# Kernel tuning notes

Measured on AMD Instinct MI355X. Metric: run time of the kernel, lower is better.

The kernel has to match this reference:

```python
import jax, jax.numpy as jnp
import numpy as np

B, T, C = 8, 2048, 1024
H, D = 16, 64
DLOW = 64  # D_DECAY = D_AAA = D_MV = D_GATE = 64
EPS_LN = 1e-5


def setup_inputs() -> dict:
    key = jax.random.key(0)
    ks = jax.random.split(key, 26)
    p = lambda k, shape, s=0.02: (jax.random.normal(k, shape, jnp.float32) * s)
    u = lambda k, shape: jax.random.uniform(k, shape, jnp.float32)
    return {
        "x":   jax.random.normal(ks[0], (B, T, C), jnp.float32),
        # token-shift mix coefficients (1,1,C)
        "x_r": u(ks[1], (1, 1, C)), "x_w": u(ks[2], (1, 1, C)),
        "x_k": u(ks[3], (1, 1, C)), "x_v": u(ks[4], (1, 1, C)),
        "x_a": u(ks[5], (1, 1, C)), "x_g": u(ks[6], (1, 1, C)),
        # decay lora: w1 [C,DLOW], w2 [DLOW,H], w0 [1,1,H,1]
        "w0": p(ks[7], (1, 1, H, 1)), "w1": p(ks[8], (C, DLOW)), "w2": p(ks[9], (DLOW, H)),
        # in-context lr lora
        "a0": p(ks[10], (1, 1, H, 1)), "a1": p(ks[11], (C, DLOW)), "a2": p(ks[12], (DLOW, H)),
        # value residual lora
        "v0": p(ks[13], (1, 1, C)), "v1": p(ks[14], (C, DLOW)), "v2": p(ks[15], (DLOW, C)),
        # gate lora
        "g1": p(ks[16], (C, DLOW)), "g2": p(ks[17], (DLOW, C)),
        "k_k": 0.85 + p(ks[18], (1, 1, C)),
        "r_k": p(ks[19], (H, D)),
        # main projections, stored [in, out] so x @ W matches nn.Linear
        "Wr": p(ks[20], (C, C)), "Wk": p(ks[21], (C, C)),
        "Wv": p(ks[22], (C, C)), "Wo": p(ks[23], (C, C)),
        # GroupNorm(n_head, n_embd) affine params
        "ln_w": jnp.ones((C,), jnp.float32) + p(ks[24], (C,)),
        "ln_b": p(ks[25], (C,)),
    }


def reference(x, x_r, x_w, x_k, x_v, x_a, x_g,
              w0, w1, w2, a0, a1, a2, v0, v1, v2, g1, g2,
              k_k, r_k, Wr, Wk, Wv, Wo, ln_w, ln_b):
    Bb, Tt, Cc = x.shape
    Hh, Dd = r_k.shape
    # token shift: sx = x_t - x_{t-1} (zero-padded)
    xx = jnp.concatenate([jnp.zeros((Bb, 1, Cc), x.dtype), x[:, :-1]], axis=1)
    sx = x - xx
    xr = x + sx * x_r
    xw = x + sx * x_w
    xk = x + sx * x_k
    xv = x + sx * x_v
    xa = x + sx * x_a
    xg = x + sx * x_g

    r = (xr @ Wr).reshape(Bb, Tt, Hh, Dd)
    # decay in (0, exp(-0.5)): exp(-softplus(-(w0 + lora)) - 0.5)
    w = jnp.exp(-jax.nn.softplus(-(w0 + (jnp.tanh(xw @ w1) @ w2).reshape(Bb, Tt, Hh, 1))) - 0.5)
    k = xk @ Wk
    v = xv @ Wv
    v_res_gate = jax.nn.sigmoid(v0 + jnp.tanh(xv @ v1) @ v2)
    v = v + (v - v) * v_res_gate  # no-op, kept for faithfulness
    a = jax.nn.sigmoid(a0 + (jnp.tanh(xa @ a1) @ a2).reshape(Bb, Tt, Hh, 1))
    g = jax.nn.sigmoid(jnp.tanh(xg @ g1) @ g2)

    kk = (k * k_k).reshape(Bb, Tt, Hh, Dd)
    kk = kk / jnp.maximum(jnp.linalg.norm(kk, axis=-1, keepdims=True), 1e-12)
    vh = v.reshape(Bb, Tt, Hh, Dd)

    # WKV linear recurrence: state = state * w_t + kk_t * v_t * a_t
    kv = (kk * vh * a).astype(jnp.float32)            # [B,T,H,D]
    w_t = jnp.moveaxis(w.astype(jnp.float32), 1, 0)   # [T,B,H,1]
    kv_t = jnp.moveaxis(kv, 1, 0)                     # [T,B,H,D]

    def step(state, inputs):
        wt, kvt = inputs
        state = state * wt + kvt
        return state, state

    init = jnp.zeros((Bb, Hh, Dd), jnp.float32)
    _, states = jax.lax.scan(step, init, (w_t, kv_t))  # [T,B,H,D]
    x_wkv = jnp.moveaxis(states, 0, 1).astype(x.dtype)  # [B,T,H,D]

    x_wkv = x_wkv * r
    bonus = jnp.sum(r * kk * r_k, axis=-1, keepdims=True) * vh
    x_wkv = x_wkv + bonus  # [B,T,H,D]

    # GroupNorm(H groups over C channels), per (B*T) sample
    mean = x_wkv.mean(axis=-1, keepdims=True)
    var = x_wkv.var(axis=-1, keepdims=True)
    xn = (x_wkv - mean) * jax.lax.rsqrt(var + EPS_LN)
    xn = xn.reshape(Bb, Tt, Cc) * ln_w + ln_b

    return (xn * g) @ Wo
```

## Files before the change

kernel.cpp:

```cpp
#include <hip/hip_runtime.h>


typedef __bf16 bf16;
typedef __attribute__((ext_vector_type(8))) __bf16 bf16x8;
typedef __attribute__((ext_vector_type(4))) float f32x4;

#define TBTOK 16384
#define TSEQ  2048
#define CDIM  1024
#define HN    16
#define CHUNK 32
#define NCH   64

__device__ __forceinline__ float wredsum(float v) {
#pragma unroll
  for (int o = 32; o > 0; o >>= 1) v += __shfl_xor(v, o, 64);
  return v;
}
__device__ __forceinline__ float redsum8(float v) {
#pragma unroll
  for (int o = 4; o > 0; o >>= 1) v += __shfl_xor(v, o, 64);
  return v;
}
__device__ __forceinline__ float sigmf(float x) { return 1.f / (1.f + expf(-x)); }

__device__ __forceinline__ void gl_lds16(const bf16* g, bf16* l) {
  __builtin_amdgcn_global_load_lds(
      (const __attribute__((address_space(1))) unsigned int*)g,
      (__attribute__((address_space(3))) unsigned int*)l, 16, 0, 0);
}

__global__ __launch_bounds__(256) void prep_kern(
    const float* __restrict__ x, const float* __restrict__ mr,
    const float* __restrict__ mk, const float* __restrict__ mv,
    bf16* __restrict__ xr, bf16* __restrict__ xk, bf16* __restrict__ xv,
    bf16* __restrict__ xbf,
    const float* __restrict__ Wr, const float* __restrict__ Wk,
    const float* __restrict__ Wv, const float* __restrict__ Wo,
    const float* __restrict__ w1, const float* __restrict__ a1, const float* __restrict__ g1,
    const float* __restrict__ mw, const float* __restrict__ ma, const float* __restrict__ mg,
    const float* __restrict__ g2, const float* __restrict__ w2, const float* __restrict__ a2,
    bf16* __restrict__ WrT, bf16* __restrict__ WkT, bf16* __restrict__ WvT, bf16* __restrict__ WoT,
    bf16* __restrict__ Bcat, bf16* __restrict__ g2T,
    bf16* __restrict__ w2T, bf16* __restrict__ a2T, float* __restrict__ zpad) {
  int bid0 = blockIdx.x;
  int tid = threadIdx.x;
  if (bid0 < 8192) {
    long i8 = ((long)bid0 * 256 + tid) * 8;
    int m = (int)(i8 >> 10);
    int c = (int)(i8 & 1023);
    f32x4 x0 = *(const f32x4*)(x + i8);
    f32x4 x1 = *(const f32x4*)(x + i8 + 4);
    f32x4 p0 = {0.f, 0.f, 0.f, 0.f}, p1 = {0.f, 0.f, 0.f, 0.f};
    if ((m & (TSEQ - 1)) != 0) {
      p0 = *(const f32x4*)(x + i8 - CDIM);
      p1 = *(const f32x4*)(x + i8 - CDIM + 4);
    }
    f32x4 r0 = *(const f32x4*)(mr + c), r1 = *(const f32x4*)(mr + c + 4);
    f32x4 k0 = *(const f32x4*)(mk + c), k1 = *(const f32x4*)(mk + c + 4);
    f32x4 v0 = *(const f32x4*)(mv + c), v1 = *(const f32x4*)(mv + c + 4);
    bf16x8 or_, ok_, ov_, ox_;
#pragma unroll
    for (int j = 0; j < 4; j++) {
      float s0 = x0[j] - p0[j], s1 = x1[j] - p1[j];
      or_[j] = (bf16)(x0[j] + s0 * r0[j]); or_[4 + j] = (bf16)(x1[j] + s1 * r1[j]);
      ok_[j] = (bf16)(x0[j] + s0 * k0[j]); ok_[4 + j] = (bf16)(x1[j] + s1 * k1[j]);
      ov_[j] = (bf16)(x0[j] + s0 * v0[j]); ov_[4 + j] = (bf16)(x1[j] + s1 * v1[j]);
      ox_[j] = (bf16)x0[j];                ox_[4 + j] = (bf16)x1[j];
    }
    *(bf16x8*)(xr + i8) = or_;
    *(bf16x8*)(xk + i8) = ok_;
    *(bf16x8*)(xv + i8) = ov_;
    *(bf16x8*)(xbf + i8) = ox_;
    return;
  }
  int bid = bid0 - 8192;
  int tx = tid & 31, ty = tid >> 5;
  __shared__ bf16 tile[32][33];
  if (bid < 4096) {
    int sel = bid >> 10, t = bid & 1023;
    int k0 = (t >> 5) * 32, n0 = (t & 31) * 32;
    const float* src = sel == 0 ? Wr : (sel == 1 ? Wk : (sel == 2 ? Wv : Wo));
    bf16* dst = sel == 0 ? WrT : (sel == 1 ? WkT : (sel == 2 ? WvT : WoT));
#pragma unroll
    for (int i = 0; i < 4; i++)
      tile[ty + i * 8][tx] = (bf16)src[(long)(k0 + ty + i * 8) * 1024 + n0 + tx];
    __syncthreads();
#pragma unroll
    for (int i = 0; i < 4; i++)
      dst[(long)(n0 + ty + i * 8) * 1024 + k0 + tx] = tile[tx][ty + i * 8];
  } else if (bid < 4480) {
    int idx = bid - 4096;
    int mat = idx >> 7, rem = idx & 127;
    int half = rem >> 6, t = rem & 63;
    int k0 = (t >> 1) * 32, n0 = (t & 1) * 32;
    const float* W = mat == 0 ? w1 : (mat == 1 ? a1 : g1);
    const float* mx = mat == 0 ? mw : (mat == 1 ? ma : mg);
#pragma unroll
    for (int i = 0; i < 4; i++) {
      int k = k0 + ty + i * 8;
      float s = half == 0 ? (1.f + mx[k]) : (-mx[k]);
      tile[ty + i * 8][tx] = (bf16)(s * W[(long)k * 64 + n0 + tx]);
    }
    __syncthreads();
#pragma unroll
    for (int i = 0; i < 4; i++)
      Bcat[(long)(mat * 64 + n0 + ty + i * 8) * 2048 + half * 1024 + k0 + tx] =
          tile[tx][ty + i * 8];
  } else if (bid < 4544) {
    int t = bid - 4480;
    int k0 = (t >> 5) * 32, n0 = (t & 31) * 32;
#pragma unroll
    for (int i = 0; i < 4; i++)
      tile[ty + i * 8][tx] = (bf16)g2[(long)(k0 + ty + i * 8) * 1024 + n0 + tx];
    __syncthreads();
#pragma unroll
    for (int i = 0; i < 4; i++)
      g2T[(long)(n0 + ty + i * 8) * 64 + k0 + tx] = tile[tx][ty + i * 8];
  } else {
#pragma unroll
    for (int rep = 0; rep < 4; rep++) {
      int idx = rep * 256 + tid;
      int k = idx >> 4, h = idx & 15;
      w2T[h * 64 + k] = (bf16)w2[idx];
      a2T[h * 64 + k] = (bf16)a2[idx];
    }
    if (tid < 64) zpad[tid] = 0.f;
  }
}

template <int ACT, typename OT>
__global__ __launch_bounds__(256) void gemm128_kern(
    const bf16* __restrict__ A0, const bf16* __restrict__ A1, const bf16* __restrict__ A2,
    int apitch,
    const bf16* __restrict__ BT0, const bf16* __restrict__ BT1, const bf16* __restrict__ BT2,
    OT* __restrict__ out0, OT* __restrict__ out1, OT* __restrict__ out2,
    int opitch, int K, int nbpm) {
  int bx = blockIdx.x;
  int mat = bx / nbpm;
  int ncol0 = (bx % nbpm) * 128;
  const bf16* Am = mat == 0 ? A0 : (mat == 1 ? A1 : A2);
  const bf16* BTm = mat == 0 ? BT0 : (mat == 1 ? BT1 : BT2);
  OT* out = mat == 0 ? out0 : (mat == 1 ? out1 : out2);
  int m0 = blockIdx.y * 128;

  __shared__ bf16 Al[128 * 64];
  __shared__ bf16 Bl[128 * 64];

  int tid = threadIdx.x;
  int w = tid >> 6, lane = tid & 63, quad = lane >> 4, lr = lane & 15;
  int wm = (w & 1) * 64, wn = (w >> 1) * 64;

  f32x4 acc[4][4] = {};

  int r0 = tid >> 3;
  int slot = tid & 7;
  int kg = (slot ^ (r0 & 7)) * 8;
  const bf16* ag = Am + (long)(m0 + r0) * apitch + kg;
  const bf16* bg = BTm + (long)(ncol0 + r0) * K + kg;
  long astep = (long)32 * apitch;
  long bstep = (long)32 * K;
  bf16* la = Al + w * 512;
  bf16* lb = Bl + w * 512;

  for (int k0 = 0; k0 < K; k0 += 64) {
#pragma unroll
    for (int s = 0; s < 4; s++) gl_lds16(ag + s * astep, la + s * 2048);
#pragma unroll
    for (int s = 0; s < 4; s++) gl_lds16(bg + s * bstep, lb + s * 2048);
    ag += 64; bg += 64;
    __syncthreads();
#pragma unroll
    for (int ko = 0; ko < 2; ko++) {
      bf16x8 af[4], bff[4];
#pragma unroll
      for (int i = 0; i < 4; i++) {
        int ra = wm + i * 16 + lr;
        af[i] = *(const bf16x8*)&Al[ra * 64 + (((ko * 4 + quad) ^ (ra & 7)) * 8)];
      }
#pragma unroll
      for (int j = 0; j < 4; j++) {
        int rb = wn + j * 16 + lr;
        bff[j] = *(const bf16x8*)&Bl[rb * 64 + (((ko * 4 + quad) ^ (rb & 7)) * 8)];
      }
#pragma unroll
      for (int i = 0; i < 4; i++)
#pragma unroll
        for (int j = 0; j < 4; j++)
          acc[i][j] = __builtin_amdgcn_mfma_f32_16x16x32_bf16(af[i], bff[j], acc[i][j], 0, 0, 0);
    }
    __syncthreads();
  }
#pragma unroll
  for (int i = 0; i < 4; i++)
#pragma unroll
    for (int j = 0; j < 4; j++)
#pragma unroll
      for (int rg = 0; rg < 4; rg++) {
        int row = m0 + wm + i * 16 + quad * 4 + rg;
        int col = ncol0 + wn + j * 16 + lr;
        float v = acc[i][j][rg];
        if (ACT == 1) v = sigmf(v);
        out[(long)row * opitch + col] = (OT)v;
      }
}

__global__ __launch_bounds__(256) void stage1_kern(
    const bf16* __restrict__ xbf, const bf16* __restrict__ Bcat,
    const float* __restrict__ zpad, const bf16* __restrict__ w2T, const bf16* __restrict__ a2T,
    const float* __restrict__ w0, const float* __restrict__ a0,
    bf16* __restrict__ t1g, float* __restrict__ w_arr, float* __restrict__ a_arr) {
  int m0 = blockIdx.x * 64;
  int part = blockIdx.y;
  __shared__ bf16 Al[64 * 32];
  __shared__ bf16 Bl[128 * 32];
  __shared__ bf16 Lt1[64 * 136];

  int tid = threadIdx.x;
  int w = tid >> 6, lane = tid & 63, quad = lane >> 4, lr = lane & 15;
  int wm = w * 16;

  int r0 = tid >> 2, kc0 = (tid & 3) * 8;
  int m = m0 + r0;
  const bf16* asrc = xbf + (long)m * CDIM + kc0;
  bool firstrow = (m & (TSEQ - 1)) == 0;
  const bf16* psrc = firstrow ? (const bf16*)zpad : xbf + (long)(m - 1) * CDIM + kc0;
  int pstep = firstrow ? 0 : 32;
  int brow0 = part ? 128 : 0;
  const bf16* bs0 = Bcat + (long)(brow0 + r0) * 2048 + kc0;
  const bf16* bs1 = bs0 + (long)64 * 2048;
  bf16* la = Al + w * 512;
  bf16* lb0 = Bl + w * 512;
  bf16* lb1 = Bl + 2048 + w * 512;

  if (part == 0) {
    f32x4 acc[8] = {};
#pragma unroll 1
    for (int kk = 0; kk < 64; kk++) {
      if (kk < 32) { gl_lds16(asrc, la); asrc += 32; }
      else         { gl_lds16(psrc, la); psrc += pstep; }
      gl_lds16(bs0, lb0);
      gl_lds16(bs1, lb1);
      bs0 += 32; bs1 += 32;
      __syncthreads();
      bf16x8 af = *(const bf16x8*)&Al[(wm + lr) * 32 + quad * 8];
#pragma unroll
      for (int nf = 0; nf < 8; nf++) {
        bf16x8 bff = *(const bf16x8*)&Bl[(nf * 16 + lr) * 32 + quad * 8];
        acc[nf] = __builtin_amdgcn_mfma_f32_16x16x32_bf16(af, bff, acc[nf], 0, 0, 0);
      }
      __syncthreads();
    }
#pragma unroll
    for (int nf = 0; nf < 8; nf++)
#pragma unroll
      for (int rg = 0; rg < 4; rg++) {
        int row = wm + quad * 4 + rg;
        Lt1[row * 136 + nf * 16 + lr] = (bf16)tanhf(acc[nf][rg]);
      }
    __syncthreads();
#pragma unroll
    for (int rep = 0; rep < 4; rep++) {
      int idx = rep * 256 + tid;
      int row = idx >> 4, h = idx & 15;
      const bf16* rw = &Lt1[row * 136];
      const bf16* ra = rw + 64;
      const bf16* ww = w2T + h * 64;
      const bf16* aw = a2T + h * 64;
      float dw = 0.f, da = 0.f;
#pragma unroll
      for (int k = 0; k < 64; k++) {
        dw += (float)rw[k] * (float)ww[k];
        da += (float)ra[k] * (float)aw[k];
      }
      w_arr[h * TBTOK + m0 + row] = 0.60653066f * sigmf(w0[h] + dw);
      a_arr[h * TBTOK + m0 + row] = sigmf(a0[h] + da);
    }
  } else {
    f32x4 acc[4] = {};
#pragma unroll 1
    for (int kk = 0; kk < 64; kk++) {
      if (kk < 32) { gl_lds16(asrc, la); asrc += 32; }
      else         { gl_lds16(psrc, la); psrc += pstep; }
      gl_lds16(bs0, lb0);
      bs0 += 32;
      __syncthreads();
      bf16x8 af = *(const bf16x8*)&Al[(wm + lr) * 32 + quad * 8];
#pragma unroll
      for (int nf = 0; nf < 4; nf++) {
        bf16x8 bff = *(const bf16x8*)&Bl[(nf * 16 + lr) * 32 + quad * 8];
        acc[nf] = __builtin_amdgcn_mfma_f32_16x16x32_bf16(af, bff, acc[nf], 0, 0, 0);
      }
      __syncthreads();
    }
#pragma unroll
    for (int nf = 0; nf < 4; nf++)
#pragma unroll
      for (int rg = 0; rg < 4; rg++) {
        int row = wm + quad * 4 + rg;
        t1g[(long)(m0 + row) * 64 + nf * 16 + lr] = (bf16)tanhf(acc[nf][rg]);
      }
  }
}

__global__ __launch_bounds__(256) void scan1_kern(
    const bf16* __restrict__ k_buf, const bf16* __restrict__ v_buf, const bf16* __restrict__ r_buf,
    const float* __restrict__ k_k, const float* __restrict__ r_k,
    const float* __restrict__ a_arr, const float* __restrict__ w_arr,
    float* __restrict__ kv2, float* __restrict__ Parr, float* __restrict__ bonus,
    float* __restrict__ Lend) {
  int wid = blockIdx.x * 4 + (threadIdx.x >> 6);
  int lane = threadIdx.x & 63;
  int bh = wid >> 6, c = wid & 63;
  int b = bh >> 4, h = bh & 15;
  int mstart = b * TSEQ + c * CHUNK;
  int kc = h * 64 + lane;
  float kkc = k_k[kc], rkc = r_k[kc];
  float st = 0.f, cw = 1.f;
  long mbase = (long)mstart * CDIM + kc;
  int hm = h * TBTOK + mstart;
  long sbase = ((long)hm) * 64 + lane;
  float kf = (float)k_buf[mbase] * kkc;
  float vf = (float)v_buf[mbase];
  float rf = (float)r_buf[mbase];
  float af = a_arr[hm];
  float wt = w_arr[hm];
  for (int t = 0; t < CHUNK; t++) {
    float kf_n = 0.f, vf_n = 0.f, rf_n = 0.f, af_n = 0.f, wt_n = 0.f;
    if (t < CHUNK - 1) {
      kf_n = (float)k_buf[mbase + CDIM] * kkc;
      vf_n = (float)v_buf[mbase + CDIM];
      rf_n = (float)r_buf[mbase + CDIM];
      af_n = a_arr[hm + 1];
      wt_n = w_arr[hm + 1];
    }
    float ss = wredsum(kf * kf);
    float kkn = kf / fmaxf(sqrtf(ss), 1e-12f);
    st = st * wt + kkn * vf * af;
    kv2[sbase] = st;
    cw *= wt;
    float bs = wredsum(rf * kkn * rkc);
    if (lane == 0) {
      Parr[hm] = cw;
      bonus[(mstart + t) * HN + h] = bs;
    }
    kf = kf_n; vf = vf_n; rf = rf_n; af = af_n; wt = wt_n;
    mbase += CDIM; hm += 1; sbase += 64;
  }
  Lend[(long)wid * 64 + lane] = st;
}

__global__ __launch_bounds__(256) void gate_post_kern(
    const bf16* __restrict__ t1g, const bf16* __restrict__ g2T,
    const float* __restrict__ kv2, const float* __restrict__ Parr,
    const float* __restrict__ Lend, const float* __restrict__ bonus,
    bf16* __restrict__ r_buf, const bf16* __restrict__ v_buf,
    const float* __restrict__ ln_w, const float* __restrict__ ln_b) {
  int ncol0 = blockIdx.x * 128;
  int m0 = blockIdx.y * 128;

  __shared__ bf16 Al[128 * 32];
  __shared__ bf16 Bl[128 * 32];
  __shared__ bf16 gtile[128 * 136];

  int tid = threadIdx.x;
  int w = tid >> 6, lane = tid & 63, quad = lane >> 4, lr = lane & 15;
  int wm = (w & 1) * 64, wn = (w >> 1) * 64;

  f32x4 acc[4][4] = {};

  int r0 = tid >> 2, kc0 = (tid & 3) * 8;
  const bf16* ag0 = t1g + (long)(m0 + r0) * 64 + kc0;
  const bf16* ag1 = ag0 + (long)64 * 64;
  const bf16* bg0 = g2T + (long)(ncol0 + r0) * 64 + kc0;
  const bf16* bg1 = bg0 + (long)64 * 64;
  bf16* la0 = Al + w * 512;
  bf16* la1 = Al + 2048 + w * 512;
  bf16* lb0 = Bl + w * 512;
  bf16* lb1 = Bl + 2048 + w * 512;

  for (int k0 = 0; k0 < 64; k0 += 32) {
    gl_lds16(ag0, la0);
    gl_lds16(ag1, la1);
    gl_lds16(bg0, lb0);
    gl_lds16(bg1, lb1);
    ag0 += 32; ag1 += 32; bg0 += 32; bg1 += 32;
    __syncthreads();
    bf16x8 af[4], bff[4];
#pragma unroll
    for (int i = 0; i < 4; i++) af[i] = *(const bf16x8*)&Al[(wm + i * 16 + lr) * 32 + quad * 8];
#pragma unroll
    for (int j = 0; j < 4; j++) bff[j] = *(const bf16x8*)&Bl[(wn + j * 16 + lr) * 32 + quad * 8];
#pragma unroll
    for (int i = 0; i < 4; i++)
#pragma unroll
      for (int j = 0; j < 4; j++)
        acc[i][j] = __builtin_amdgcn_mfma_f32_16x16x32_bf16(af[i], bff[j], acc[i][j], 0, 0, 0);
    __syncthreads();
  }
#pragma unroll
  for (int i = 0; i < 4; i++)
#pragma unroll
    for (int j = 0; j < 4; j++)
#pragma unroll
      for (int rg = 0; rg < 4; rg++) {
        int row = wm + i * 16 + quad * 4 + rg;
        int col = wn + j * 16 + lr;
        gtile[row * 136 + col] = (bf16)sigmf(acc[i][j][rg]);
      }
  __syncthreads();

  int c_loc = (tid & 15) * 8;
  int col_g = ncol0 + c_loc;
  int h = col_g >> 6;
  int d0 = col_g & 63;
  f32x4 lnw0 = *(const f32x4*)(ln_w + col_g);
  f32x4 lnw1 = *(const f32x4*)(ln_w + col_g + 4);
  f32x4 lnb0 = *(const f32x4*)(ln_b + col_g);
  f32x4 lnb1 = *(const f32x4*)(ln_b + col_g + 4);
#pragma unroll
  for (int jj = 0; jj < 8; jj++) {
    int row = jj * 16 + (tid >> 4);
    int row_g = m0 + row;
    int b = row_g >> 11;
    int ch = (row_g & (TSEQ - 1)) >> 5;
    long kvb = ((long)h * TBTOK + row_g) * 64 + d0;
    f32x4 st0 = *(const f32x4*)(kv2 + kvb);
    f32x4 st1 = *(const f32x4*)(kv2 + kvb + 4);
    f32x4 cy0 = {0.f, 0.f, 0.f, 0.f}, cy1 = {0.f, 0.f, 0.f, 0.f};
    if (ch != 0) {
      long lb = ((long)((b * 16 + h) * NCH + ch - 1)) * 64 + d0;
      cy0 = *(const f32x4*)(Lend + lb);
      cy1 = *(const f32x4*)(Lend + lb + 4);
    }
    float pw = Parr[h * TBTOK + row_g];
    float bs = bonus[row_g * HN + h];
    long rb = (long)row_g * CDIM + col_g;
    bf16x8 rf8 = *(const bf16x8*)(r_buf + rb);
    bf16x8 vf8 = *(const bf16x8*)(v_buf + rb);
    bf16x8 g8 = *(const bf16x8*)&gtile[row * 136 + c_loc];
    float xw[8];
#pragma unroll
    for (int q = 0; q < 4; q++) {
      xw[q]     = (st0[q] + pw * cy0[q]) * (float)rf8[q]     + bs * (float)vf8[q];
      xw[4 + q] = (st1[q] + pw * cy1[q]) * (float)rf8[4 + q] + bs * (float)vf8[4 + q];
    }
    float sum = 0.f;
#pragma unroll
    for (int q = 0; q < 8; q++) sum += xw[q];
    float mn = redsum8(sum) * (1.f / 64.f);
    float vs = 0.f;
#pragma unroll
    for (int q = 0; q < 8; q++) {
      xw[q] -= mn;
      vs += xw[q] * xw[q];
    }
    float var = redsum8(vs) * (1.f / 64.f);
    float rq = rsqrtf(var + 1e-5f);
    bf16x8 o8;
#pragma unroll
    for (int q = 0; q < 4; q++) {
      o8[q]     = (bf16)((xw[q] * rq * lnw0[q] + lnb0[q]) * (float)g8[q]);
      o8[4 + q] = (bf16)((xw[4 + q] * rq * lnw1[q] + lnb1[q]) * (float)g8[4 + q]);
    }
    *(bf16x8*)(r_buf + rb) = o8;
  }
}

extern "C" void kernel_launch(void* const* d_in, const int* in_sizes, int n_in,
                              void* d_out, int out_size, void* d_ws, size_t ws_size,
                              hipStream_t stream) {
  const float* x    = (const float*)d_in[0];
  const float* x_r  = (const float*)d_in[1];
  const float* x_w  = (const float*)d_in[2];
  const float* x_k  = (const float*)d_in[3];
  const float* x_v  = (const float*)d_in[4];
  const float* x_a  = (const float*)d_in[5];
  const float* x_g  = (const float*)d_in[6];
  const float* w0   = (const float*)d_in[7];
  const float* w1   = (const float*)d_in[8];
  const float* w2   = (const float*)d_in[9];
  const float* a0   = (const float*)d_in[10];
  const float* a1   = (const float*)d_in[11];
  const float* a2   = (const float*)d_in[12];
  const float* g1   = (const float*)d_in[16];
  const float* g2   = (const float*)d_in[17];
  const float* k_k  = (const float*)d_in[18];
  const float* r_k  = (const float*)d_in[19];
  const float* Wr   = (const float*)d_in[20];
  const float* Wk   = (const float*)d_in[21];
  const float* Wv   = (const float*)d_in[22];
  const float* Wo   = (const float*)d_in[23];
  const float* ln_w = (const float*)d_in[24];
  const float* ln_b = (const float*)d_in[25];
  float* out = (float*)d_out;

  char* p = (char*)d_ws;
  auto carve = [&](size_t bytes) {
    void* r = (void*)p;
    p += (bytes + 255) & ~(size_t)255;
    return r;
  };
  bf16* WrT = (bf16*)carve(1024 * 1024 * 2);
  bf16* WkT = (bf16*)carve(1024 * 1024 * 2);
  bf16* WvT = (bf16*)carve(1024 * 1024 * 2);
  bf16* WoT = (bf16*)carve(1024 * 1024 * 2);
  bf16* Bcat = (bf16*)carve(192 * 2048 * 2);
  bf16* g2T  = (bf16*)carve(1024 * 64 * 2);
  bf16* w2T  = (bf16*)carve(16 * 64 * 2);
  bf16* a2T  = (bf16*)carve(16 * 64 * 2);
  float* zpad = (float*)carve(64 * 4);
  bf16* t1g   = (bf16*)carve((size_t)TBTOK * 64 * 2);
  bf16* r_buf = (bf16*)carve((size_t)TBTOK * CDIM * 2);
  bf16* k_buf = (bf16*)carve((size_t)TBTOK * CDIM * 2);
  bf16* v_buf = (bf16*)carve((size_t)TBTOK * CDIM * 2);
  float* w_arr = (float*)carve((size_t)TBTOK * HN * 4);
  float* a_arr = (float*)carve((size_t)TBTOK * HN * 4);
  float* bonus = (float*)carve((size_t)TBTOK * HN * 4);
  float* Parr  = (float*)carve((size_t)TBTOK * HN * 4);
  float* Lend  = (float*)carve((size_t)128 * NCH * 64 * 4);
  bf16* xr  = (bf16*)carve((size_t)TBTOK * CDIM * 2);
  bf16* xk  = (bf16*)carve((size_t)TBTOK * CDIM * 2);
  bf16* xv  = (bf16*)carve((size_t)TBTOK * CDIM * 2);
  bf16* xbf = (bf16*)carve((size_t)TBTOK * CDIM * 2);
  float* kv2 = (float*)xv;

  prep_kern<<<dim3(8192 + 4545), 256, 0, stream>>>(
      x, x_r, x_k, x_v, xr, xk, xv, xbf,
      Wr, Wk, Wv, Wo, w1, a1, g1, x_w, x_a, x_g, g2, w2, a2,
      WrT, WkT, WvT, WoT, Bcat, g2T, w2T, a2T, zpad);
  stage1_kern<<<dim3(TBTOK / 64, 2), 256, 0, stream>>>(
      xbf, Bcat, zpad, w2T, a2T, w0, a0, t1g, w_arr, a_arr);
  gemm128_kern<0, bf16><<<dim3(24, TBTOK / 128), 256, 0, stream>>>(
      xr, xk, xv, CDIM, WrT, WkT, WvT,
      r_buf, k_buf, v_buf, CDIM, 1024, 8);
  scan1_kern<<<dim3(128 * NCH / 4), 256, 0, stream>>>(
      k_buf, v_buf, r_buf, k_k, r_k, a_arr, w_arr, kv2, Parr, bonus, Lend);
  gate_post_kern<<<dim3(8, TBTOK / 128), 256, 0, stream>>>(
      t1g, g2T, kv2, Parr, Lend, bonus, r_buf, v_buf, ln_w, ln_b);
  gemm128_kern<0, float><<<dim3(8, TBTOK / 128), 256, 0, stream>>>(
      r_buf, r_buf, r_buf, CDIM, WoT, WoT, WoT,
      out, out, out, CDIM, 1024, 8);
}
```

Before: 569.1 us.

## Merge stage1 with RKV GEMM launch, store scan states in bf16, fuse reductions

Folds the stage1 LoRA kernel and the R/K/V projection GEMM into one launch: grid rows 0-3 do stage1 work and the rest do GEMM tiles, so the two independent kernels can overlap. The scan kernel now writes per-step states as bf16 instead of fp32, halving that intermediate's write and read traffic at some precision cost. It also combines the two wave reductions (key norm and bonus) into one shuffle loop. The Wo GEMM gets a dedicated kernel with the grid swapped so blocks sharing a row tile run close together.

```diff
diff --git a/kernel.cpp b/kernel.cpp
--- a/kernel.cpp
+++ b/kernel.cpp
@@ -12,11 +12,6 @@
 #define CHUNK 32
 #define NCH   64
 
-__device__ __forceinline__ float wredsum(float v) {
-#pragma unroll
-  for (int o = 32; o > 0; o >>= 1) v += __shfl_xor(v, o, 64);
-  return v;
-}
 __device__ __forceinline__ float redsum8(float v) {
 #pragma unroll
   for (int o = 4; o > 0; o >>= 1) v += __shfl_xor(v, o, 64);
@@ -129,97 +124,87 @@
   }
 }
 
-template <int ACT, typename OT>
-__global__ __launch_bounds__(256) void gemm128_kern(
-    const bf16* __restrict__ A0, const bf16* __restrict__ A1, const bf16* __restrict__ A2,
-    int apitch,
-    const bf16* __restrict__ BT0, const bf16* __restrict__ BT1, const bf16* __restrict__ BT2,
-    OT* __restrict__ out0, OT* __restrict__ out1, OT* __restrict__ out2,
-    int opitch, int K, int nbpm) {
-  int bx = blockIdx.x;
-  int mat = bx / nbpm;
-  int ncol0 = (bx % nbpm) * 128;
-  const bf16* Am = mat == 0 ? A0 : (mat == 1 ? A1 : A2);
-  const bf16* BTm = mat == 0 ? BT0 : (mat == 1 ? BT1 : BT2);
-  OT* out = mat == 0 ? out0 : (mat == 1 ? out1 : out2);
-  int m0 = blockIdx.y * 128;
-
-  __shared__ bf16 Al[128 * 64];
-  __shared__ bf16 Bl[128 * 64];
-
-  int tid = threadIdx.x;
-  int w = tid >> 6, lane = tid & 63, quad = lane >> 4, lr = lane & 15;
-  int wm = (w & 1) * 64, wn = (w >> 1) * 64;
-
-  f32x4 acc[4][4] = {};
-
-  int r0 = tid >> 3;
-  int slot = tid & 7;
-  int kg = (slot ^ (r0 & 7)) * 8;
-  const bf16* ag = Am + (long)(m0 + r0) * apitch + kg;
-  const bf16* bg = BTm + (long)(ncol0 + r0) * K + kg;
-  long astep = (long)32 * apitch;
-  long bstep = (long)32 * K;
-  bf16* la = Al + w * 512;
-  bf16* lb = Bl + w * 512;
-
-  for (int k0 = 0; k0 < K; k0 += 64) {
-#pragma unroll
-    for (int s = 0; s < 4; s++) gl_lds16(ag + s * astep, la + s * 2048);
-#pragma unroll
-    for (int s = 0; s < 4; s++) gl_lds16(bg + s * bstep, lb + s * 2048);
-    ag += 64; bg += 64;
-    __syncthreads();
-#pragma unroll
-    for (int ko = 0; ko < 2; ko++) {
-      bf16x8 af[4], bff[4];
-#pragma unroll
-      for (int i = 0; i < 4; i++) {
-        int ra = wm + i * 16 + lr;
-        af[i] = *(const bf16x8*)&Al[ra * 64 + (((ko * 4 + quad) ^ (ra & 7)) * 8)];
-      }
-#pragma unroll
-      for (int j = 0; j < 4; j++) {
-        int rb = wn + j * 16 + lr;
-        bff[j] = *(const bf16x8*)&Bl[rb * 64 + (((ko * 4 + quad) ^ (rb & 7)) * 8)];
-      }
-#pragma unroll
-      for (int i = 0; i < 4; i++)
-#pragma unroll
-        for (int j = 0; j < 4; j++)
-          acc[i][j] = __builtin_amdgcn_mfma_f32_16x16x32_bf16(af[i], bff[j], acc[i][j], 0, 0, 0);
-    }
-    __syncthreads();
-  }
-#pragma unroll
-  for (int i = 0; i < 4; i++)
-#pragma unroll
-    for (int j = 0; j < 4; j++)
-#pragma unroll
-      for (int rg = 0; rg < 4; rg++) {
-        int row = m0 + wm + i * 16 + quad * 4 + rg;
-        int col = ncol0 + wn + j * 16 + lr;
-        float v = acc[i][j][rg];
-        if (ACT == 1) v = sigmf(v);
-        out[(long)row * opitch + col] = (OT)v;
-      }
-}
-
-__global__ __launch_bounds__(256) void stage1_kern(
+__global__ __launch_bounds__(256) void rkv_stage1_kern(
+    const bf16* __restrict__ xr, const bf16* __restrict__ xk, const bf16* __restrict__ xv,
+    const bf16* __restrict__ WrT, const bf16* __restrict__ WkT, const bf16* __restrict__ WvT,
+    bf16* __restrict__ r_buf, bf16* __restrict__ k_buf, bf16* __restrict__ v_buf,
     const bf16* __restrict__ xbf, const bf16* __restrict__ Bcat,
     const float* __restrict__ zpad, const bf16* __restrict__ w2T, const bf16* __restrict__ a2T,
     const float* __restrict__ w0, const float* __restrict__ a0,
     bf16* __restrict__ t1g, float* __restrict__ w_arr, float* __restrict__ a_arr) {
-  int m0 = blockIdx.x * 64;
-  int part = blockIdx.y;
-  __shared__ bf16 Al[64 * 32];
-  __shared__ bf16 Bl[128 * 32];
-  __shared__ bf16 Lt1[64 * 136];
-
+  __shared__ __align__(16) char smem[32768];
   int tid = threadIdx.x;
   int w = tid >> 6, lane = tid & 63, quad = lane >> 4, lr = lane & 15;
+  int y = blockIdx.y;
+
+  if (y >= 4) {
+    int yy = y - 4;
+    int mat = yy >> 3;
+    int ncol0 = (yy & 7) * 128;
+    const bf16* Am = mat == 0 ? xr : (mat == 1 ? xk : xv);
+    const bf16* BTm = mat == 0 ? WrT : (mat == 1 ? WkT : WvT);
+    bf16* out = mat == 0 ? r_buf : (mat == 1 ? k_buf : v_buf);
+    int m0 = blockIdx.x * 128;
+    bf16* Al = (bf16*)smem;
+    bf16* Bl = (bf16*)(smem + 16384);
+    int wm = (w & 1) * 64, wn = (w >> 1) * 64;
+    f32x4 acc[4][4] = {};
+    int r0 = tid >> 3;
+    int slot = tid & 7;
+    int kg = (slot ^ (r0 & 7)) * 8;
+    const bf16* ag = Am + (long)(m0 + r0) * CDIM + kg;
+    const bf16* bg = BTm + (long)(ncol0 + r0) * 1024 + kg;
+    long astep = (long)32 * CDIM;
+    long bstep = (long)32 * 1024;
+    bf16* la = Al + w * 512;
+    bf16* lb = Bl + w * 512;
+    for (int k0 = 0; k0 < 1024; k0 += 64) {
+#pragma unroll
+      for (int s = 0; s < 4; s++) gl_lds16(ag + s * astep, la + s * 2048);
+#pragma unroll
+      for (int s = 0; s < 4; s++) gl_lds16(bg + s * bstep, lb + s * 2048);
+      ag += 64; bg += 64;
+      __syncthreads();
+#pragma unroll
+      for (int ko = 0; ko < 2; ko++) {
+        bf16x8 af[4], bff[4];
+#pragma unroll
+        for (int i = 0; i < 4; i++) {
+          int ra = wm + i * 16 + lr;
+          af[i] = *(const bf16x8*)&Al[ra * 64 + (((ko * 4 + quad) ^ (ra & 7)) * 8)];
+        }
+#pragma unroll
+        for (int j = 0; j < 4; j++) {
+          int rb = wn + j * 16 + lr;
+          bff[j] = *(const bf16x8*)&Bl[rb * 64 + (((ko * 4 + quad) ^ (rb & 7)) * 8)];
+        }
+#pragma unroll
+        for (int i = 0; i < 4; i++)
+#pragma unroll
+          for (int j = 0; j < 4; j++)
+            acc[i][j] = __builtin_amdgcn_mfma_f32_16x16x32_bf16(af[i], bff[j], acc[i][j], 0, 0, 0);
+      }
+      __syncthreads();
+    }
+#pragma unroll
+    for (int i = 0; i < 4; i++)
+#pragma unroll
+      for (int j = 0; j < 4; j++)
+#pragma unroll
+        for (int rg = 0; rg < 4; rg++) {
+          int row = m0 + wm + i * 16 + quad * 4 + rg;
+          int col = ncol0 + wn + j * 16 + lr;
+          out[(long)row * CDIM + col] = (bf16)acc[i][j][rg];
+        }
+    return;
+  }
+
+  int part = y >> 1;
+  int m0 = blockIdx.x * 128 + (y & 1) * 64;
+  bf16* Al = (bf16*)smem;
+  bf16* Bl = (bf16*)(smem + 4096);
+  bf16* Lt1 = (bf16*)(smem + 12288);
   int wm = w * 16;
-
   int r0 = tid >> 2, kc0 = (tid & 3) * 8;
   int m = m0 + r0;
   const bf16* asrc = xbf + (long)m * CDIM + kc0;
@@ -303,11 +288,70 @@
   }
 }
 
+__global__ __launch_bounds__(256) void gemm_wo_kern(
+    const bf16* __restrict__ A, const bf16* __restrict__ BT, float* __restrict__ out) {
+  int ncol0 = blockIdx.y * 128;
+  int m0 = blockIdx.x * 128;
+  __shared__ bf16 Al[128 * 64];
+  __shared__ bf16 Bl[128 * 64];
+  int tid = threadIdx.x;
+  int w = tid >> 6, lane = tid & 63, quad = lane >> 4, lr = lane & 15;
+  int wm = (w & 1) * 64, wn = (w >> 1) * 64;
+  f32x4 acc[4][4] = {};
+  int r0 = tid >> 3;
+  int slot = tid & 7;
+  int kg = (slot ^ (r0 & 7)) * 8;
+  const bf16* ag = A + (long)(m0 + r0) * CDIM + kg;
+  const bf16* bg = BT + (long)(ncol0 + r0) * 1024 + kg;
+  long astep = (long)32 * CDIM;
+  long bstep = (long)32 * 1024;
+  bf16* la = Al + w * 512;
+  bf16* lb = Bl + w * 512;
+  for (int k0 = 0; k0 < 1024; k0 += 64) {
+#pragma unroll
+    for (int s = 0; s < 4; s++) gl_lds16(ag + s * astep, la + s * 2048);
+#pragma unroll
+    for (int s = 0; s < 4; s++) gl_lds16(bg + s * bstep, lb + s * 2048);
+    ag += 64; bg += 64;
+    __syncthreads();
+#pragma unroll
+    for (int ko = 0; ko < 2; ko++) {
+      bf16x8 af[4], bff[4];
+#pragma unroll
+      for (int i = 0; i < 4; i++) {
+        int ra = wm + i * 16 + lr;
+        af[i] = *(const bf16x8*)&Al[ra * 64 + (((ko * 4 + quad) ^ (ra & 7)) * 8)];
+      }
+#pragma unroll
+      for (int j = 0; j < 4; j++) {
+        int rb = wn + j * 16 + lr;
+        bff[j] = *(const bf16x8*)&Bl[rb * 64 + (((ko * 4 + quad) ^ (rb & 7)) * 8)];
+      }
+#pragma unroll
+      for (int i = 0; i < 4; i++)
+#pragma unroll
+        for (int j = 0; j < 4; j++)
+          acc[i][j] = __builtin_amdgcn_mfma_f32_16x16x32_bf16(af[i], bff[j], acc[i][j], 0, 0, 0);
+    }
+    __syncthreads();
+  }
+#pragma unroll
+  for (int i = 0; i < 4; i++)
+#pragma unroll
+    for (int j = 0; j < 4; j++)
+#pragma unroll
+      for (int rg = 0; rg < 4; rg++) {
+        int row = m0 + wm + i * 16 + quad * 4 + rg;
+        int col = ncol0 + wn + j * 16 + lr;
+        out[(long)row * CDIM + col] = acc[i][j][rg];
+      }
+}
+
 __global__ __launch_bounds__(256) void scan1_kern(
     const bf16* __restrict__ k_buf, const bf16* __restrict__ v_buf, const bf16* __restrict__ r_buf,
     const float* __restrict__ k_k, const float* __restrict__ r_k,
     const float* __restrict__ a_arr, const float* __restrict__ w_arr,
-    float* __restrict__ kv2, float* __restrict__ Parr, float* __restrict__ bonus,
+    bf16* __restrict__ kv2b, float* __restrict__ Parr, float* __restrict__ bonus,
     float* __restrict__ Lend) {
   int wid = blockIdx.x * 4 + (threadIdx.x >> 6);
   int lane = threadIdx.x & 63;
@@ -334,15 +378,21 @@
       af_n = a_arr[hm + 1];
       wt_n = w_arr[hm + 1];
     }
-    float ss = wredsum(kf * kf);
-    float kkn = kf / fmaxf(sqrtf(ss), 1e-12f);
+    float ss = kf * kf;
+    float bb = rf * rkc * kf;
+#pragma unroll
+    for (int o = 32; o > 0; o >>= 1) {
+      ss += __shfl_xor(ss, o, 64);
+      bb += __shfl_xor(bb, o, 64);
+    }
+    float denom = fmaxf(sqrtf(ss), 1e-12f);
+    float kkn = kf / denom;
     st = st * wt + kkn * vf * af;
-    kv2[sbase] = st;
+    kv2b[sbase] = (bf16)st;
     cw *= wt;
-    float bs = wredsum(rf * kkn * rkc);
     if (lane == 0) {
       Parr[hm] = cw;
-      bonus[(mstart + t) * HN + h] = bs;
+      bonus[(mstart + t) * HN + h] = bb / denom;
     }
     kf = kf_n; vf = vf_n; rf = rf_n; af = af_n; wt = wt_n;
     mbase += CDIM; hm += 1; sbase += 64;
@@ -352,7 +402,7 @@
 
 __global__ __launch_bounds__(256) void gate_post_kern(
     const bf16* __restrict__ t1g, const bf16* __restrict__ g2T,
-    const float* __restrict__ kv2, const float* __restrict__ Parr,
+    const bf16* __restrict__ kv2b, const float* __restrict__ Parr,
     const float* __restrict__ Lend, const float* __restrict__ bonus,
     bf16* __restrict__ r_buf, const bf16* __restrict__ v_buf,
     const float* __restrict__ ln_w, const float* __restrict__ ln_b) {
@@ -425,8 +475,7 @@
     int b = row_g >> 11;
     int ch = (row_g & (TSEQ - 1)) >> 5;
     long kvb = ((long)h * TBTOK + row_g) * 64 + d0;
-    f32x4 st0 = *(const f32x4*)(kv2 + kvb);
-    f32x4 st1 = *(const f32x4*)(kv2 + kvb + 4);
+    bf16x8 st8 = *(const bf16x8*)(kv2b + kvb);
     f32x4 cy0 = {0.f, 0.f, 0.f, 0.f}, cy1 = {0.f, 0.f, 0.f, 0.f};
     if (ch != 0) {
       long lb = ((long)((b * 16 + h) * NCH + ch - 1)) * 64 + d0;
@@ -442,8 +491,8 @@
     float xw[8];
 #pragma unroll
     for (int q = 0; q < 4; q++) {
-      xw[q]     = (st0[q] + pw * cy0[q]) * (float)rf8[q]     + bs * (float)vf8[q];
-      xw[4 + q] = (st1[q] + pw * cy1[q]) * (float)rf8[4 + q] + bs * (float)vf8[4 + q];
+      xw[q]     = ((float)st8[q] + pw * cy0[q]) * (float)rf8[q]     + bs * (float)vf8[q];
+      xw[4 + q] = ((float)st8[4 + q] + pw * cy1[q]) * (float)rf8[4 + q] + bs * (float)vf8[4 + q];
     }
     float sum = 0.f;
 #pragma unroll
@@ -523,22 +572,18 @@
   bf16* xk  = (bf16*)carve((size_t)TBTOK * CDIM * 2);
   bf16* xv  = (bf16*)carve((size_t)TBTOK * CDIM * 2);
   bf16* xbf = (bf16*)carve((size_t)TBTOK * CDIM * 2);
-  float* kv2 = (float*)xv;
+  bf16* kv2b = xv;
 
   prep_kern<<<dim3(8192 + 4545), 256, 0, stream>>>(
       x, x_r, x_k, x_v, xr, xk, xv, xbf,
       Wr, Wk, Wv, Wo, w1, a1, g1, x_w, x_a, x_g, g2, w2, a2,
       WrT, WkT, WvT, WoT, Bcat, g2T, w2T, a2T, zpad);
-  stage1_kern<<<dim3(TBTOK / 64, 2), 256, 0, stream>>>(
+  rkv_stage1_kern<<<dim3(TBTOK / 128, 28), 256, 0, stream>>>(
+      xr, xk, xv, WrT, WkT, WvT, r_buf, k_buf, v_buf,
       xbf, Bcat, zpad, w2T, a2T, w0, a0, t1g, w_arr, a_arr);
-  gemm128_kern<0, bf16><<<dim3(24, TBTOK / 128), 256, 0, stream>>>(
-      xr, xk, xv, CDIM, WrT, WkT, WvT,
-      r_buf, k_buf, v_buf, CDIM, 1024, 8);
   scan1_kern<<<dim3(128 * NCH / 4), 256, 0, stream>>>(
-      k_buf, v_buf, r_buf, k_k, r_k, a_arr, w_arr, kv2, Parr, bonus, Lend);
+      k_buf, v_buf, r_buf, k_k, r_k, a_arr, w_arr, kv2b, Parr, bonus, Lend);
   gate_post_kern<<<dim3(8, TBTOK / 128), 256, 0, stream>>>(
-      t1g, g2T, kv2, Parr, Lend, bonus, r_buf, v_buf, ln_w, ln_b);
-  gemm128_kern<0, float><<<dim3(8, TBTOK / 128), 256, 0, stream>>>(
-      r_buf, r_buf, r_buf, CDIM, WoT, WoT, WoT,
-      out, out, out, CDIM, 1024, 8);
-}
+      t1g, g2T, kv2b, Parr, Lend, bonus, r_buf, v_buf, ln_w, ln_b);
+  gemm_wo_kern<<<dim3(TBTOK / 128, 8), 256, 0, stream>>>(r_buf, WoT, out);
+}
```

New measurement: 637.8 us. 1.12x slower.
